# Optimization experiments

Measured on AMD Instinct MI355X. Metric: run time of the kernel, lower is better.

## Reference

```python
import jax, jax.numpy as jnp
import numpy as np

PAD = 20  # (41 - 1) // 2, matches ReflectionPad2d(20)
CHANNELS = 6


def _matlab_gauss2d(shape=(41, 41), sigma=10.0):
    m, n = [(s - 1.0) / 2.0 for s in shape]
    y, x = np.ogrid[-m:m + 1, -n:n + 1]
    h = np.exp(-(x * x + y * y) / (2.0 * sigma * sigma))
    h[h < np.finfo(h.dtype).eps * h.max()] = 0
    s = h.sum()
    if s != 0:
        h /= s
    return h


def setup_inputs() -> dict:
    key = jax.random.key(0)
    x = jax.random.normal(key, (16, CHANNELS, 512, 512), dtype=jnp.float32)
    k = _matlab_gauss2d((41, 41), 10.0)  # [41, 41]
    # depthwise weight [C, 1, 41, 41], same kernel repeated per channel
    weight = jnp.asarray(np.repeat(k[None, None], CHANNELS, axis=0), dtype=jnp.float32)
    return {"x": x, "weight": weight}


def reference(x, weight):
    # reflect-pad H and W by 20 (PyTorch ReflectionPad2d semantics == jnp 'reflect')
    xp = jnp.pad(x, ((0, 0), (0, 0), (PAD, PAD), (PAD, PAD)), mode="reflect")
    # depthwise conv: feature_group_count = C, weight is [C, 1, kH, kW]
    out = jax.lax.conv_general_dilated(
        xp, weight,
        window_strides=(1, 1),
        padding="VALID",
        dimension_numbers=("NCHW", "OIHW", "NCHW"),
        feature_group_count=CHANNELS,
    )
    return out  # [B, C, H, W]
```

## Files before the change

### kernel.cpp

```cpp
#include <hip/hip_runtime.h>

#define KS 41
#define PAD 20
#define H 512
#define W 512
#define CH 6
#define PROW 552

__device__ __forceinline__ int reflect_idx(int i, int n) {
    if (i < 0) i = -i;
    if (i >= n) i = 2 * n - 2 - i;
    return i;
}

__device__ __forceinline__ int reflect511(int i) {
    return (H - 1) - abs((H - 1) - abs(i));
}

__device__ __forceinline__ float uniform_f(float v) {
    return __uint_as_float(__builtin_amdgcn_readfirstlane(__float_as_uint(v)));
}

__device__ __forceinline__ void load_coeffs(const float* __restrict__ w, int c,
                                            int lane, float gk[KS]) {
    float my = 0.f;
    if (lane < KS) {
        const float* wr = w + (size_t)c * KS * KS + (size_t)lane * KS;
        #pragma unroll
        for (int j = 0; j < KS; ++j) my += wr[j];
    }
    #pragma unroll
    for (int j = 0; j < KS; ++j)
        gk[j] = __uint_as_float(__builtin_amdgcn_readlane(__float_as_uint(my), j));
}

__global__ __launch_bounds__(256, 6)
void gauss_h_kernel(const float* __restrict__ x, const float* __restrict__ w,
                    float* __restrict__ ws) {
    __shared__ float rb[4][PROW];

    const int tid = threadIdx.x;
    const int wv  = tid >> 6;
    const int l   = tid & 63;
    const int img = blockIdx.y;
    const int c   = img % CH;
    const int row = blockIdx.x * 4 + wv;

    const float* rp = x + ((size_t)img * H + row) * W;
    const float4 v0 = ((const float4*)rp)[l];
    const float4 v1 = ((const float4*)rp)[l + 64];

    float gk[KS];
    load_coeffs(w, c, l, gk);

    float* L = rb[wv];
    *(float4*)(L + PAD + 4 * l)        = v0;
    *(float4*)(L + PAD + 4 * (l + 64)) = v1;
    __builtin_amdgcn_wave_barrier();

    if (l < 2 * PAD) {
        const int dstp = (l < PAD) ? l        : (512 + l);
        const int srcp = (l < PAD) ? (40 - l) : (550 - l);
        L[dstp] = L[srcp];
    }
    __builtin_amdgcn_wave_barrier();

    float* op = ws + ((size_t)img * H + row) * W;

    #pragma unroll
    for (int hh = 0; hh < 2; ++hh) {
        const int c0 = 256 * hh + 4 * l;
        const float* Lw = L + c0;
        float a0 = 0.f, a1 = 0.f, a2 = 0.f, a3 = 0.f;

        #pragma unroll
        for (int m = 0; m < 11; ++m) {
            const float4 q = *(const float4*)(Lw + 4 * m);
            const float f[4] = {q.x, q.y, q.z, q.w};
            #pragma unroll
            for (int t = 0; t < 4; ++t) {
                const int k = 4 * m + t;
                if (k <= 40)            a0 += gk[k]     * f[t];
                if (k >= 1 && k <= 41)  a1 += gk[k - 1] * f[t];
                if (k >= 2 && k <= 42)  a2 += gk[k - 2] * f[t];
                if (k >= 3)             a3 += gk[k - 3] * f[t];
            }
        }
        *(float4*)(op + c0) = make_float4(a0, a1, a2, a3);
    }
}

#define VTW 64
#define VTH 128
#define VTMPH (VTH + 2 * PAD)

__global__ __launch_bounds__(256, 3)
void gauss_v_kernel(const float* __restrict__ ws, const float* __restrict__ w,
                    float* __restrict__ out) {
    __shared__ float tmp[VTMPH * VTW];

    const int tid = threadIdx.x;
    const int bx  = blockIdx.x;
    const int by  = blockIdx.y;
    const int img = blockIdx.z;
    const int c   = img % CH;

    float gk[KS];
    load_coeffs(w, c, tid & 63, gk);

    const float* sbase = ws + (size_t)img * H * W + bx * VTW;
    for (int idx = tid; idx < VTMPH * 16; idx += 256) {
        const int r  = idx >> 4;
        const int q  = idx & 15;
        const int sr = reflect511(by * VTH - PAD + r);
        float4 v = *(const float4*)(sbase + (size_t)sr * W + 4 * q);
        *(float4*)&tmp[r * VTW + 4 * q] = v;
    }
    __syncthreads();

    const int lx = tid & 63;
    const int yg = tid >> 6;
    float* o = out + ((size_t)img * H + by * VTH) * W + bx * VTW + lx;

    #pragma unroll
    for (int cc = 0; cc < 2; ++cc) {
        const int yc = yg * 32 + cc * 16;
        float col[56];
        #pragma unroll
        for (int i = 0; i < 56; ++i)
            col[i] = tmp[(yc + i) * VTW + lx];
        #pragma unroll
        for (int y = 0; y < 16; ++y) {
            float s = 0.f;
            #pragma unroll
            for (int j = 0; j < KS; ++j) s += gk[j] * col[y + j];
            o[(size_t)(yc + y) * W] = s;
        }
    }
}

#define TW 64
#define TH 128
#define TMPH (TH + 2 * PAD)

__global__ __launch_bounds__(256, 3)
void gauss_blur_fused_kernel(const float* __restrict__ x,
                             const float* __restrict__ w,
                             float* __restrict__ out) {
    __shared__ float g_s[KS];
    __shared__ float tmp[TMPH * TW];

    const int tid = threadIdx.x;
    const int bx = blockIdx.x, by = blockIdx.y, bz = blockIdx.z;
    const int c = bz % CH;

    if (tid < KS) {
        const float* wr = w + (size_t)c * KS * KS + (size_t)tid * KS;
        float s = 0.f;
        #pragma unroll
        for (int j = 0; j < KS; ++j) s += wr[j];
        g_s[tid] = s;
    }
    __syncthreads();

    float gr[KS];
    #pragma unroll
    for (int j = 0; j < KS; ++j) gr[j] = uniform_f(g_s[j]);

    const size_t img_off = (size_t)bz * (H * W);
    const float* img = x + img_off;
    const int x_tile = bx * TW;

    for (int gid = tid; gid < TMPH * (TW / 8); gid += 256) {
        const int r  = gid >> 3;
        const int gx = gid & 7;
        const int gy = reflect_idx(by * TH - PAD + r, H);
        const int x0 = x_tile + gx * 8;
        const float* row = img + (size_t)gy * W;

        float s[8];
        #pragma unroll
        for (int k = 0; k < 8; ++k) s[k] = 0.f;

        if (x0 >= PAD && x0 + 27 <= W - 1) {
            const float4* p = (const float4*)(row + x0 - PAD);
            #pragma unroll
            for (int m = 0; m < 12; ++m) {
                const float4 v = p[m];
                const float f[4] = {v.x, v.y, v.z, v.w};
                #pragma unroll
                for (int t = 0; t < 4; ++t) {
                    const int pos = 4 * m + t;
                    #pragma unroll
                    for (int k = 0; k < 8; ++k) {
                        const int tap = pos - k;
                        if (tap >= 0 && tap < KS) s[k] += gr[tap] * f[t];
                    }
                }
            }
        } else {
            #pragma unroll
            for (int pos = 0; pos < 48; ++pos) {
                const float f = row[reflect_idx(x0 - PAD + pos, W)];
                #pragma unroll
                for (int k = 0; k < 8; ++k) {
                    const int tap = pos - k;
                    if (tap >= 0 && tap < KS) s[k] += gr[tap] * f;
                }
            }
        }
        float* dstp = &tmp[r * TW + gx * 8];
        #pragma unroll
        for (int k = 0; k < 8; ++k) dstp[k] = s[k];
    }
    __syncthreads();

    const int lx = tid & 63;
    const int yg = tid >> 6;
    float* o = out + img_off;

    #pragma unroll
    for (int cc = 0; cc < 2; ++cc) {
        const int yc = yg * 32 + cc * 16;
        float col[56];
        #pragma unroll
        for (int i = 0; i < 56; ++i)
            col[i] = tmp[(yc + i) * TW + lx];
        #pragma unroll
        for (int y = 0; y < 16; ++y) {
            float s = 0.f;
            #pragma unroll
            for (int j = 0; j < KS; ++j) s += gr[j] * col[y + j];
            o[(size_t)(by * TH + yc + y) * W + x_tile + lx] = s;
        }
    }
}

extern "C" void kernel_launch(void* const* d_in, const int* in_sizes, int n_in,
                              void* d_out, int out_size, void* d_ws, size_t ws_size,
                              hipStream_t stream) {
    const float* x = (const float*)d_in[0];
    const float* w = (const float*)d_in[1];
    float* out = (float*)d_out;
    (void)in_sizes; (void)n_in; (void)out_size;

    const size_t need = (size_t)16 * CH * H * W * sizeof(float);
    if (ws_size >= need) {
        float* ws = (float*)d_ws;
        gauss_h_kernel<<<dim3(H / 4, 16 * CH), 256, 0, stream>>>(x, w, ws);
        gauss_v_kernel<<<dim3(W / VTW, H / VTH, 16 * CH), 256, 0, stream>>>(ws, w, out);
    } else {
        dim3 grid(W / TW, H / TH, 16 * CH);
        gauss_blur_fused_kernel<<<grid, 256, 0, stream>>>(x, w, out);
    }
}
```

Baseline: 253.0 us.

## Replace separate H/V blur kernels with one transpose-and-blur kernel run twice

Swaps the row-wise horizontal kernel and the tiled vertical kernel for a single kernel. It loads a reflected tile into shared memory transposed (padded stride 65), convolves along columns in registers, and writes the result transposed. Running it twice gives a separable blur with correct orientation, and both passes share the register-resident column convolution. In exchange, the tile loads become scalar, uncoalesced-per-column writes into LDS and the global stores become transposed. It also reads the reflect-padded halo in both passes.

```diff
diff --git a/kernel.cpp b/kernel.cpp
--- a/kernel.cpp
+++ b/kernel.cpp
@@ -5,7 +5,13 @@
 #define H 512
 #define W 512
 #define CH 6
-#define PROW 552
+
+#define TR 64
+#define TC 128
+#define PC (TC + 2 * PAD)
+#define LSTR 65
+#define WCOL 32
+#define CWIN (WCOL + 2 * PAD)
 
 __device__ __forceinline__ int reflect_idx(int i, int n) {
     if (i < 0) i = -i;
@@ -34,108 +40,44 @@
         gk[j] = __uint_as_float(__builtin_amdgcn_readlane(__float_as_uint(my), j));
 }
 
-__global__ __launch_bounds__(256, 6)
-void gauss_h_kernel(const float* __restrict__ x, const float* __restrict__ w,
-                    float* __restrict__ ws) {
-    __shared__ float rb[4][PROW];
+__global__ __launch_bounds__(256, 3)
+void hblurT_kernel(const float* __restrict__ in, const float* __restrict__ w,
+                   float* __restrict__ outT) {
+    __shared__ float tmp[PC * LSTR];
 
     const int tid = threadIdx.x;
     const int wv  = tid >> 6;
     const int l   = tid & 63;
-    const int img = blockIdx.y;
+    const int img = blockIdx.z;
     const int c   = img % CH;
-    const int row = blockIdx.x * 4 + wv;
-
-    const float* rp = x + ((size_t)img * H + row) * W;
-    const float4 v0 = ((const float4*)rp)[l];
-    const float4 v1 = ((const float4*)rp)[l + 64];
+    const int c0  = blockIdx.x * TC;
+    const int r0  = blockIdx.y * TR;
 
     float gk[KS];
     load_coeffs(w, c, l, gk);
 
-    float* L = rb[wv];
-    *(float4*)(L + PAD + 4 * l)        = v0;
-    *(float4*)(L + PAD + 4 * (l + 64)) = v1;
-    __builtin_amdgcn_wave_barrier();
-
-    if (l < 2 * PAD) {
-        const int dstp = (l < PAD) ? l        : (512 + l);
-        const int srcp = (l < PAD) ? (40 - l) : (550 - l);
-        L[dstp] = L[srcp];
-    }
-    __builtin_amdgcn_wave_barrier();
-
-    float* op = ws + ((size_t)img * H + row) * W;
-
+    const float* ip = in + (size_t)img * H * W;
     #pragma unroll
-    for (int hh = 0; hh < 2; ++hh) {
-        const int c0 = 256 * hh + 4 * l;
-        const float* Lw = L + c0;
-        float a0 = 0.f, a1 = 0.f, a2 = 0.f, a3 = 0.f;
-
-        #pragma unroll
-        for (int m = 0; m < 11; ++m) {
-            const float4 q = *(const float4*)(Lw + 4 * m);
-            const float f[4] = {q.x, q.y, q.z, q.w};
-            #pragma unroll
-            for (int t = 0; t < 4; ++t) {
-                const int k = 4 * m + t;
-                if (k <= 40)            a0 += gk[k]     * f[t];
-                if (k >= 1 && k <= 41)  a1 += gk[k - 1] * f[t];
-                if (k >= 2 && k <= 42)  a2 += gk[k - 2] * f[t];
-                if (k >= 3)             a3 += gk[k - 3] * f[t];
-            }
-        }
-        *(float4*)(op + c0) = make_float4(a0, a1, a2, a3);
-    }
-}
-
-#define VTW 64
-#define VTH 128
-#define VTMPH (VTH + 2 * PAD)
-
-__global__ __launch_bounds__(256, 3)
-void gauss_v_kernel(const float* __restrict__ ws, const float* __restrict__ w,
-                    float* __restrict__ out) {
-    __shared__ float tmp[VTMPH * VTW];
-
-    const int tid = threadIdx.x;
-    const int bx  = blockIdx.x;
-    const int by  = blockIdx.y;
-    const int img = blockIdx.z;
-    const int c   = img % CH;
-
-    float gk[KS];
-    load_coeffs(w, c, tid & 63, gk);
-
-    const float* sbase = ws + (size_t)img * H * W + bx * VTW;
-    for (int idx = tid; idx < VTMPH * 16; idx += 256) {
-        const int r  = idx >> 4;
-        const int q  = idx & 15;
-        const int sr = reflect511(by * VTH - PAD + r);
-        float4 v = *(const float4*)(sbase + (size_t)sr * W + 4 * q);
-        *(float4*)&tmp[r * VTW + 4 * q] = v;
+    for (int k = 0; k < (TR * PC) / 256; ++k) {
+        const int t = k * 256 + tid;
+        const int r = t / PC;
+        const int p = t - r * PC;
+        tmp[p * LSTR + r] = ip[(size_t)(r0 + r) * W + reflect511(c0 - PAD + p)];
     }
     __syncthreads();
 
-    const int lx = tid & 63;
-    const int yg = tid >> 6;
-    float* o = out + ((size_t)img * H + by * VTH) * W + bx * VTW + lx;
+    float col[CWIN];
+    #pragma unroll
+    for (int i = 0; i < CWIN; ++i)
+        col[i] = tmp[(WCOL * wv + i) * LSTR + l];
 
+    float* op = outT + (size_t)img * H * W + (size_t)(c0 + WCOL * wv) * H + r0 + l;
     #pragma unroll
-    for (int cc = 0; cc < 2; ++cc) {
-        const int yc = yg * 32 + cc * 16;
-        float col[56];
+    for (int u = 0; u < WCOL; ++u) {
+        float s = 0.f;
         #pragma unroll
-        for (int i = 0; i < 56; ++i)
-            col[i] = tmp[(yc + i) * VTW + lx];
-        #pragma unroll
-        for (int y = 0; y < 16; ++y) {
-            float s = 0.f;
-            #pragma unroll
-            for (int j = 0; j < KS; ++j) s += gk[j] * col[y + j];
-            o[(size_t)(yc + y) * W] = s;
-        }
+        for (int j = 0; j < KS; ++j) s += gk[j] * col[u + j];
+        op[(size_t)u * H] = s;
     }
 }
 
@@ -247,8 +189,9 @@
     const size_t need = (size_t)16 * CH * H * W * sizeof(float);
     if (ws_size >= need) {
         float* ws = (float*)d_ws;
-        gauss_h_kernel<<<dim3(H / 4, 16 * CH), 256, 0, stream>>>(x, w, ws);
-        gauss_v_kernel<<<dim3(W / VTW, H / VTH, 16 * CH), 256, 0, stream>>>(ws, w, out);
+        const dim3 grid(W / TC, H / TR, 16 * CH);
+        hblurT_kernel<<<grid, 256, 0, stream>>>(x,  w, ws);
+        hblurT_kernel<<<grid, 256, 0, stream>>>(ws, w, out);
     } else {
         dim3 grid(W / TW, H / TH, 16 * CH);
         gauss_blur_fused_kernel<<<grid, 256, 0, stream>>>(x, w, out);
```

New measurement: 245.5 us. 3.0% less time.
